# Performance work log

Measured on AMD Instinct MI355X. Metric: run time of the kernel, lower is better.

Reference implementation:

```python
import jax, jax.numpy as jnp
import numpy as np

N_NODES = 100000
N_EDGES = 1600000
NFEAT, NHID, NCLASS = 512, 128, 16


def gcn_conv(x, edge_index, edge_weight, W, b):
    # Dense linear transform: [N, in] @ [in, out] -> [N, out]
    h = x @ W
    src, dst = edge_index[0], edge_index[1]
    # Edge-weighted gather + scatter-add (message passing)
    msgs = edge_weight[:, None] * h[src]            # [E, out]
    agg = jax.ops.segment_sum(msgs, dst, num_segments=x.shape[0])
    return agg + b


def setup_inputs() -> dict:
    key = jax.random.key(0)
    k = jax.random.split(key, 8)
    x = jax.random.normal(k[0], (N_NODES, NFEAT), dtype=jnp.float32)
    edge_index = jax.random.randint(k[1], (2, N_EDGES), 0, N_NODES, dtype=jnp.int64 if jax.config.jax_enable_x64 else jnp.int32)
    edge_weight = jax.random.uniform(k[2], (N_EDGES,), dtype=jnp.float32)
    # GCNConv glorot-initialized weights + zero biases
    s1 = np.sqrt(6.0 / (NFEAT + NHID)).astype(np.float32)
    s2 = np.sqrt(6.0 / (NHID + NCLASS)).astype(np.float32)
    W1 = jax.random.uniform(k[3], (NFEAT, NHID), minval=-s1, maxval=s1, dtype=jnp.float32)
    b1 = jnp.zeros((NHID,), dtype=jnp.float32)
    W2 = jax.random.uniform(k[4], (NHID, NCLASS), minval=-s2, maxval=s2, dtype=jnp.float32)
    b2 = jnp.zeros((NCLASS,), dtype=jnp.float32)
    return {"x": x, "edge_index": edge_index, "edge_weight": edge_weight,
            "W1": W1, "b1": b1, "W2": W2, "b2": b2}


def reference(x, edge_index, edge_weight, W1, b1, W2, b2):
    # GNNGuard.forward in eval mode (dropout is identity when not training)
    h = jax.nn.relu(gcn_conv(x, edge_index, edge_weight, W1, b1))
    out = gcn_conv(h, edge_index, edge_weight, W2, b2)
    return jax.nn.log_softmax(out, axis=1)
```

## Files before the change

### kernel.cpp

```cpp
#include <hip/hip_runtime.h>
#include <cstdint>
#include <cstddef>


#define NFEAT 512
#define NHID 128
#define NCLASS 16
#define MAXDEG 64

typedef __attribute__((ext_vector_type(8))) __bf16 bf16x8;
typedef __attribute__((ext_vector_type(4))) float f32x4;

__global__ void k_prep_w1(const float* __restrict__ W1, __bf16* __restrict__ W1f) {
    int t = blockIdx.x * 256 + threadIdx.x;
    if (t >= 16 * 8 * 64) return;
    int lane = t & 63;
    int nc = (t >> 6) & 7;
    int ks = t >> 9;
    int q = lane >> 4, col = lane & 15;
    __bf16* outp = W1f + (size_t)t * 8;
#pragma unroll
    for (int j = 0; j < 8; j++) {
        int k = ks * 32 + q * 8 + j;
        int n = nc * 16 + col;
        outp[j] = (__bf16)W1[k * NHID + n];
    }
}

__global__ void k_gemm1_scatter(const float* __restrict__ x, const __bf16* __restrict__ W1f,
                                __bf16* __restrict__ h1b, int M, int nG1,
                                const int* __restrict__ src, const int* __restrict__ dst,
                                const float* __restrict__ ew, int* __restrict__ cnt,
                                int2* __restrict__ pay, int E) {
    if ((int)blockIdx.x >= nG1) {
        int e = (blockIdx.x - nG1) * 256 + threadIdx.x;
        if (e < E) {
            int d = dst[e];
            int r = atomicAdd(&cnt[d], 1);
            if (r < MAXDEG) {
                int2 pv;
                pv.x = src[e];
                pv.y = __float_as_int(ew[e]);
                pay[(size_t)d * MAXDEG + r] = pv;
            }
        }
        return;
    }
    int wave = threadIdx.x >> 6;
    int lane = threadIdx.x & 63;
    int q = lane >> 4;
    int col = lane & 15;
    int m0 = blockIdx.x * 64 + wave * 16 + col;
    bool valid = (m0 < M);

    f32x4 acc[8];
#pragma unroll
    for (int n = 0; n < 8; n++) acc[n] = (f32x4)(0.0f);

    const bf16x8* Bf = (const bf16x8*)W1f;
    const float* arow = x + (size_t)m0 * NFEAT + q * 8;

    for (int kk = 0; kk < NFEAT; kk += 32) {
        bf16x8 af;
        if (valid) {
            const f32x4* ap = (const f32x4*)(arow + kk);
            f32x4 a0 = __builtin_nontemporal_load(ap);
            f32x4 a1 = __builtin_nontemporal_load(ap + 1);
            af[0] = (__bf16)a0[0]; af[1] = (__bf16)a0[1];
            af[2] = (__bf16)a0[2]; af[3] = (__bf16)a0[3];
            af[4] = (__bf16)a1[0]; af[5] = (__bf16)a1[1];
            af[6] = (__bf16)a1[2]; af[7] = (__bf16)a1[3];
        } else {
#pragma unroll
            for (int j = 0; j < 8; j++) af[j] = (__bf16)0.0f;
        }
        int kb = (kk >> 5) * 8;
#pragma unroll
        for (int n = 0; n < 8; n++) {
            bf16x8 bf = Bf[(size_t)(kb + n) * 64 + lane];
            acc[n] = __builtin_amdgcn_mfma_f32_16x16x32_bf16(af, bf, acc[n], 0, 0, 0);
        }
    }

    int rbase = blockIdx.x * 64 + wave * 16 + q * 4;
#pragma unroll
    for (int r = 0; r < 4; r++) {
        int row = rbase + r;
        if (row < M) {
            __bf16* op = h1b + (size_t)row * NHID + col;
#pragma unroll
            for (int n = 0; n < 8; n++) op[n * 16] = (__bf16)acc[n][r];
        }
    }
}

__global__ void k_agg1(const uint32_t* __restrict__ h1u, const int* __restrict__ cnt,
                       const int2* __restrict__ pay, const float* __restrict__ b1,
                       uint32_t* __restrict__ hu, int N) {
    int gw = (blockIdx.x * 256 + (int)threadIdx.x) >> 6;
    int lane = threadIdx.x & 63;
    if (gw >= N) return;
    int c = cnt[gw];
    if (c > MAXDEG) c = MAXDEG;
    const int2* prow = pay + (size_t)gw * MAXDEG;
    int sv = 0;
    float wv = 0.f;
    if (lane < c) {
        int2 pv = prow[lane];
        sv = pv.x;
        wv = __int_as_float(pv.y);
    }
    float ax = 0.f, ay = 0.f;
    int j = 0;
    for (; j + 4 <= c; j += 4) {
        int s0 = __shfl(sv, j + 0), s1 = __shfl(sv, j + 1);
        int s2 = __shfl(sv, j + 2), s3 = __shfl(sv, j + 3);
        float w0 = __shfl(wv, j + 0), w1 = __shfl(wv, j + 1);
        float w2 = __shfl(wv, j + 2), w3 = __shfl(wv, j + 3);
        uint32_t u0 = h1u[(size_t)s0 * 64 + lane];
        uint32_t u1 = h1u[(size_t)s1 * 64 + lane];
        uint32_t u2 = h1u[(size_t)s2 * 64 + lane];
        uint32_t u3 = h1u[(size_t)s3 * 64 + lane];
        ax = fmaf(w0, __uint_as_float(u0 << 16), ax);
        ay = fmaf(w0, __uint_as_float(u0 & 0xffff0000u), ay);
        ax = fmaf(w1, __uint_as_float(u1 << 16), ax);
        ay = fmaf(w1, __uint_as_float(u1 & 0xffff0000u), ay);
        ax = fmaf(w2, __uint_as_float(u2 << 16), ax);
        ay = fmaf(w2, __uint_as_float(u2 & 0xffff0000u), ay);
        ax = fmaf(w3, __uint_as_float(u3 << 16), ax);
        ay = fmaf(w3, __uint_as_float(u3 & 0xffff0000u), ay);
    }
    for (; j < c; j++) {
        int s = __shfl(sv, j);
        float ww = __shfl(wv, j);
        uint32_t u = h1u[(size_t)s * 64 + lane];
        ax = fmaf(ww, __uint_as_float(u << 16), ax);
        ay = fmaf(ww, __uint_as_float(u & 0xffff0000u), ay);
    }
    float2 bb = ((const float2*)b1)[lane];
    float ox = fmaxf(ax + bb.x, 0.f);
    float oy = fmaxf(ay + bb.y, 0.f);
    union { __bf16 h[2]; uint32_t u; } cvt;
    cvt.h[0] = (__bf16)ox;
    cvt.h[1] = (__bf16)oy;
    hu[(size_t)gw * 64 + lane] = cvt.u;
}

__global__ void k_gemm2(const uint32_t* __restrict__ hu, const float* __restrict__ W2,
                        float* __restrict__ h2, int N) {
    __shared__ float W2s[NHID * NCLASS];
    __shared__ float hs[16][NHID + 4];
    int t = threadIdx.x;
#pragma unroll
    for (int j = 0; j < 8; j++) W2s[t * 8 + j] = W2[t * 8 + j];
    int nb = blockIdx.x * 16;
    {
        int idx = t * 4;
        int row = idx >> 6;
        int kp = idx & 63;
        if (nb + row < N) {
            uint4 u4 = *(const uint4*)(hu + (size_t)(nb + row) * 64 + kp);
            uint32_t us[4] = {u4.x, u4.y, u4.z, u4.w};
#pragma unroll
            for (int j = 0; j < 4; j++) {
                hs[row][(kp + j) * 2 + 0] = __uint_as_float(us[j] << 16);
                hs[row][(kp + j) * 2 + 1] = __uint_as_float(us[j] & 0xffff0000u);
            }
        } else {
#pragma unroll
            for (int j = 0; j < 4; j++) {
                hs[row][(kp + j) * 2 + 0] = 0.f;
                hs[row][(kp + j) * 2 + 1] = 0.f;
            }
        }
    }
    __syncthreads();
    int ni = t >> 4, c = t & 15;
    float acc = 0.f;
#pragma unroll 8
    for (int k = 0; k < NHID; k++) acc = fmaf(hs[ni][k], W2s[k * NCLASS + c], acc);
    if (nb + ni < N) h2[(size_t)(nb + ni) * NCLASS + c] = acc;
}

__global__ void k_agg2(const float* __restrict__ h2, const int* __restrict__ cnt,
                       const int2* __restrict__ pay, const float* __restrict__ b2,
                       float* __restrict__ out, int N) {
    int t = blockIdx.x * 256 + threadIdx.x;
    int node = t >> 4;
    int c = t & 15;
    if (node >= N) return;
    int n = cnt[node];
    if (n > MAXDEG) n = MAXDEG;
    const int2* prow = pay + (size_t)node * MAXDEG;
    float acc = 0.f;
    int j = 0;
    for (; j + 4 <= n; j += 4) {
        int2 p0 = prow[j + 0];
        int2 p1 = prow[j + 1];
        int2 p2 = prow[j + 2];
        int2 p3 = prow[j + 3];
        float v0 = h2[(size_t)p0.x * NCLASS + c];
        float v1 = h2[(size_t)p1.x * NCLASS + c];
        float v2 = h2[(size_t)p2.x * NCLASS + c];
        float v3 = h2[(size_t)p3.x * NCLASS + c];
        acc = fmaf(__int_as_float(p0.y), v0, acc);
        acc = fmaf(__int_as_float(p1.y), v1, acc);
        acc = fmaf(__int_as_float(p2.y), v2, acc);
        acc = fmaf(__int_as_float(p3.y), v3, acc);
    }
    for (; j < n; j++) {
        int2 pv = prow[j];
        acc = fmaf(__int_as_float(pv.y), h2[(size_t)pv.x * NCLASS + c], acc);
    }
    float o = acc + b2[c];
    float m = o;
#pragma unroll
    for (int d = 1; d < 16; d <<= 1) m = fmaxf(m, __shfl_xor(m, d));
    float e = expf(o - m);
    float ssum = e;
#pragma unroll
    for (int d = 1; d < 16; d <<= 1) ssum += __shfl_xor(ssum, d);
    out[(size_t)node * NCLASS + c] = o - m - logf(ssum);
}

extern "C" void kernel_launch(void* const* d_in, const int* in_sizes, int n_in,
                              void* d_out, int out_size, void* d_ws, size_t ws_size,
                              hipStream_t stream) {
    const float* x  = (const float*)d_in[0];
    const int*   ei = (const int*)d_in[1];
    const float* ew = (const float*)d_in[2];
    const float* W1 = (const float*)d_in[3];
    const float* b1 = (const float*)d_in[4];
    const float* W2 = (const float*)d_in[5];
    const float* b2 = (const float*)d_in[6];
    float* out = (float*)d_out;

    int N = in_sizes[0] / NFEAT;
    int E = in_sizes[2];
    const int* srcI = ei;
    const int* dstI = ei + E;

    char* p = (char*)d_ws;
    auto alloc = [&](size_t bytes) {
        char* r = p;
        p += (bytes + 511) & ~(size_t)511;
        return r;
    };
    __bf16*   h1b  = (__bf16*)alloc((size_t)N * NHID * 2);
    uint32_t* hu   = (uint32_t*)alloc((size_t)N * (NHID / 2) * 4);
    float*    h2   = (float*)alloc((size_t)N * NCLASS * 4);
    int*      cnt  = (int*)alloc((size_t)N * 4);
    int2*     pay  = (int2*)alloc((size_t)N * MAXDEG * 8);
    __bf16*   W1f  = (__bf16*)alloc((size_t)NFEAT * NHID * 2);

    (void)hipMemsetAsync(cnt, 0, (size_t)N * 4, stream);
    k_prep_w1<<<32, 256, 0, stream>>>(W1, W1f);

    int nG1 = (N + 63) / 64;
    int nSc = (E + 255) / 256;
    k_gemm1_scatter<<<nG1 + nSc, 256, 0, stream>>>(x, W1f, h1b, N, nG1,
                                                   srcI, dstI, ew, cnt, pay, E);

    k_agg1<<<(N + 3) / 4, 256, 0, stream>>>((const uint32_t*)h1b, cnt, pay, b1, hu, N);
    k_gemm2<<<(N + 15) / 16, 256, 0, stream>>>(hu, W2, h2, N);
    k_agg2<<<(int)(((size_t)N * 16 + 255) / 256), 256, 0, stream>>>(h2, cnt, pay, b2, out, N);
}
```

Before: 495.5 us.

## Pad degree counters, widen GEMM tile, reorder blocks, restructure aggregation kernels

Measured after the change: 542.8 us. 1.1x slower.

```diff
diff --git a/kernel.cpp b/kernel.cpp
--- a/kernel.cpp
+++ b/kernel.cpp
@@ -7,6 +7,7 @@
 #define NHID 128
 #define NCLASS 16
 #define MAXDEG 64
+#define CNTPAD 16
 
 typedef __attribute__((ext_vector_type(8))) __bf16 bf16x8;
 typedef __attribute__((ext_vector_type(4))) float f32x4;
@@ -28,15 +29,15 @@
 }
 
 __global__ void k_gemm1_scatter(const float* __restrict__ x, const __bf16* __restrict__ W1f,
-                                __bf16* __restrict__ h1b, int M, int nG1,
+                                __bf16* __restrict__ h1b, int M, int nSc,
                                 const int* __restrict__ src, const int* __restrict__ dst,
                                 const float* __restrict__ ew, int* __restrict__ cnt,
                                 int2* __restrict__ pay, int E) {
-    if ((int)blockIdx.x >= nG1) {
-        int e = (blockIdx.x - nG1) * 256 + threadIdx.x;
+    if ((int)blockIdx.x < nSc) {
+        int e = blockIdx.x * 256 + threadIdx.x;
         if (e < E) {
             int d = dst[e];
-            int r = atomicAdd(&cnt[d], 1);
+            int r = atomicAdd(&cnt[(size_t)d * CNTPAD], 1);
             if (r < MAXDEG) {
                 int2 pv;
                 pv.x = src[e];
@@ -46,50 +47,72 @@
         }
         return;
     }
+    int bid = blockIdx.x - nSc;
     int wave = threadIdx.x >> 6;
     int lane = threadIdx.x & 63;
     int q = lane >> 4;
     int col = lane & 15;
-    int m0 = blockIdx.x * 64 + wave * 16 + col;
-    bool valid = (m0 < M);
-
-    f32x4 acc[8];
-#pragma unroll
-    for (int n = 0; n < 8; n++) acc[n] = (f32x4)(0.0f);
+    int rowbase = bid * 128 + wave * 32;
+    int m0 = rowbase + col;
+    int m1 = rowbase + 16 + col;
+    bool v0 = (m0 < M), v1 = (m1 < M);
+
+    f32x4 acc[2][8];
+#pragma unroll
+    for (int f = 0; f < 2; f++)
+#pragma unroll
+        for (int n = 0; n < 8; n++) acc[f][n] = (f32x4)(0.0f);
 
     const bf16x8* Bf = (const bf16x8*)W1f;
-    const float* arow = x + (size_t)m0 * NFEAT + q * 8;
+    const float* arow0 = x + (size_t)m0 * NFEAT + q * 8;
+    const float* arow1 = x + (size_t)m1 * NFEAT + q * 8;
 
     for (int kk = 0; kk < NFEAT; kk += 32) {
-        bf16x8 af;
-        if (valid) {
-            const f32x4* ap = (const f32x4*)(arow + kk);
+        bf16x8 af0, af1;
+        if (v0) {
+            const f32x4* ap = (const f32x4*)(arow0 + kk);
             f32x4 a0 = __builtin_nontemporal_load(ap);
             f32x4 a1 = __builtin_nontemporal_load(ap + 1);
-            af[0] = (__bf16)a0[0]; af[1] = (__bf16)a0[1];
-            af[2] = (__bf16)a0[2]; af[3] = (__bf16)a0[3];
-            af[4] = (__bf16)a1[0]; af[5] = (__bf16)a1[1];
-            af[6] = (__bf16)a1[2]; af[7] = (__bf16)a1[3];
+            af0[0] = (__bf16)a0[0]; af0[1] = (__bf16)a0[1];
+            af0[2] = (__bf16)a0[2]; af0[3] = (__bf16)a0[3];
+            af0[4] = (__bf16)a1[0]; af0[5] = (__bf16)a1[1];
+            af0[6] = (__bf16)a1[2]; af0[7] = (__bf16)a1[3];
         } else {
 #pragma unroll
-            for (int j = 0; j < 8; j++) af[j] = (__bf16)0.0f;
+            for (int j = 0; j < 8; j++) af0[j] = (__bf16)0.0f;
+        }
+        if (v1) {
+            const f32x4* ap = (const f32x4*)(arow1 + kk);
+            f32x4 a0 = __builtin_nontemporal_load(ap);
+            f32x4 a1 = __builtin_nontemporal_load(ap + 1);
+            af1[0] = (__bf16)a0[0]; af1[1] = (__bf16)a0[1];
+            af1[2] = (__bf16)a0[2]; af1[3] = (__bf16)a0[3];
+            af1[4] = (__bf16)a1[0]; af1[5] = (__bf16)a1[1];
+            af1[6] = (__bf16)a1[2]; af1[7] = (__bf16)a1[3];
+        } else {
+#pragma unroll
+            for (int j = 0; j < 8; j++) af1[j] = (__bf16)0.0f;
         }
         int kb = (kk >> 5) * 8;
 #pragma unroll
         for (int n = 0; n < 8; n++) {
             bf16x8 bf = Bf[(size_t)(kb + n) * 64 + lane];
-            acc[n] = __builtin_amdgcn_mfma_f32_16x16x32_bf16(af, bf, acc[n], 0, 0, 0);
-        }
-    }
-
-    int rbase = blockIdx.x * 64 + wave * 16 + q * 4;
-#pragma unroll
-    for (int r = 0; r < 4; r++) {
-        int row = rbase + r;
-        if (row < M) {
-            __bf16* op = h1b + (size_t)row * NHID + col;
-#pragma unroll
-            for (int n = 0; n < 8; n++) op[n * 16] = (__bf16)acc[n][r];
+            acc[0][n] = __builtin_amdgcn_mfma_f32_16x16x32_bf16(af0, bf, acc[0][n], 0, 0, 0);
+            acc[1][n] = __builtin_amdgcn_mfma_f32_16x16x32_bf16(af1, bf, acc[1][n], 0, 0, 0);
+        }
+    }
+
+#pragma unroll
+    for (int f = 0; f < 2; f++) {
+        int rb = rowbase + f * 16 + q * 4;
+#pragma unroll
+        for (int r = 0; r < 4; r++) {
+            int row = rb + r;
+            if (row < M) {
+                __bf16* op = h1b + (size_t)row * NHID + col;
+#pragma unroll
+                for (int n = 0; n < 8; n++) op[n * 16] = (__bf16)acc[f][n][r];
+            }
         }
     }
 }
@@ -100,7 +123,7 @@
     int gw = (blockIdx.x * 256 + (int)threadIdx.x) >> 6;
     int lane = threadIdx.x & 63;
     if (gw >= N) return;
-    int c = cnt[gw];
+    int c = cnt[(size_t)gw * CNTPAD];
     if (c > MAXDEG) c = MAXDEG;
     const int2* prow = pay + (size_t)gw * MAXDEG;
     int sv = 0;
@@ -112,23 +135,35 @@
     }
     float ax = 0.f, ay = 0.f;
     int j = 0;
+    for (; j + 8 <= c; j += 8) {
+        uint32_t u[8];
+        float w[8];
+#pragma unroll
+        for (int i = 0; i < 8; i++) {
+            int s = __shfl(sv, j + i);
+            w[i] = __shfl(wv, j + i);
+            u[i] = h1u[(size_t)s * 64 + lane];
+        }
+#pragma unroll
+        for (int i = 0; i < 8; i++) {
+            ax = fmaf(w[i], __uint_as_float(u[i] << 16), ax);
+            ay = fmaf(w[i], __uint_as_float(u[i] & 0xffff0000u), ay);
+        }
+    }
     for (; j + 4 <= c; j += 4) {
-        int s0 = __shfl(sv, j + 0), s1 = __shfl(sv, j + 1);
-        int s2 = __shfl(sv, j + 2), s3 = __shfl(sv, j + 3);
-        float w0 = __shfl(wv, j + 0), w1 = __shfl(wv, j + 1);
-        float w2 = __shfl(wv, j + 2), w3 = __shfl(wv, j + 3);
-        uint32_t u0 = h1u[(size_t)s0 * 64 + lane];
-        uint32_t u1 = h1u[(size_t)s1 * 64 + lane];
-        uint32_t u2 = h1u[(size_t)s2 * 64 + lane];
-        uint32_t u3 = h1u[(size_t)s3 * 64 + lane];
-        ax = fmaf(w0, __uint_as_float(u0 << 16), ax);
-        ay = fmaf(w0, __uint_as_float(u0 & 0xffff0000u), ay);
-        ax = fmaf(w1, __uint_as_float(u1 << 16), ax);
-        ay = fmaf(w1, __uint_as_float(u1 & 0xffff0000u), ay);
-        ax = fmaf(w2, __uint_as_float(u2 << 16), ax);
-        ay = fmaf(w2, __uint_as_float(u2 & 0xffff0000u), ay);
-        ax = fmaf(w3, __uint_as_float(u3 << 16), ax);
-        ay = fmaf(w3, __uint_as_float(u3 & 0xffff0000u), ay);
+        uint32_t u[4];
+        float w[4];
+#pragma unroll
+        for (int i = 0; i < 4; i++) {
+            int s = __shfl(sv, j + i);
+            w[i] = __shfl(wv, j + i);
+            u[i] = h1u[(size_t)s * 64 + lane];
+        }
+#pragma unroll
+        for (int i = 0; i < 4; i++) {
+            ax = fmaf(w[i], __uint_as_float(u[i] << 16), ax);
+            ay = fmaf(w[i], __uint_as_float(u[i] & 0xffff0000u), ay);
+        }
     }
     for (; j < c; j++) {
         int s = __shfl(sv, j);
@@ -185,33 +220,40 @@
 __global__ void k_agg2(const float* __restrict__ h2, const int* __restrict__ cnt,
                        const int2* __restrict__ pay, const float* __restrict__ b2,
                        float* __restrict__ out, int N) {
-    int t = blockIdx.x * 256 + threadIdx.x;
-    int node = t >> 4;
-    int c = t & 15;
-    if (node >= N) return;
-    int n = cnt[node];
+    int gw = (blockIdx.x * 256 + (int)threadIdx.x) >> 6;
+    int lane = threadIdx.x & 63;
+    if (gw >= N) return;
+    int c = lane & 15, eg = lane >> 4;
+    int n = cnt[(size_t)gw * CNTPAD];
     if (n > MAXDEG) n = MAXDEG;
-    const int2* prow = pay + (size_t)node * MAXDEG;
+    const int2* prow = pay + (size_t)gw * MAXDEG;
+    int sv = 0;
+    float wv = 0.f;
+    if (lane < n) {
+        int2 pv = prow[lane];
+        sv = pv.x;
+        wv = __int_as_float(pv.y);
+    }
     float acc = 0.f;
-    int j = 0;
-    for (; j + 4 <= n; j += 4) {
-        int2 p0 = prow[j + 0];
-        int2 p1 = prow[j + 1];
-        int2 p2 = prow[j + 2];
-        int2 p3 = prow[j + 3];
-        float v0 = h2[(size_t)p0.x * NCLASS + c];
-        float v1 = h2[(size_t)p1.x * NCLASS + c];
-        float v2 = h2[(size_t)p2.x * NCLASS + c];
-        float v3 = h2[(size_t)p3.x * NCLASS + c];
-        acc = fmaf(__int_as_float(p0.y), v0, acc);
-        acc = fmaf(__int_as_float(p1.y), v1, acc);
-        acc = fmaf(__int_as_float(p2.y), v2, acc);
-        acc = fmaf(__int_as_float(p3.y), v3, acc);
-    }
-    for (; j < n; j++) {
-        int2 pv = prow[j];
-        acc = fmaf(__int_as_float(pv.y), h2[(size_t)pv.x * NCLASS + c], acc);
-    }
+    int nr = (n + 3) >> 2;
+    int i = 0;
+    for (; i + 2 <= nr; i += 2) {
+        int j0 = i * 4 + eg, j1 = j0 + 4;
+        int s0 = __shfl(sv, j0), s1 = __shfl(sv, j1);
+        float w0 = __shfl(wv, j0), w1 = __shfl(wv, j1);
+        float g0 = h2[(size_t)s0 * NCLASS + c];
+        float g1 = h2[(size_t)s1 * NCLASS + c];
+        acc = fmaf(w0, g0, acc);
+        acc = fmaf(w1, g1, acc);
+    }
+    if (i < nr) {
+        int j0 = i * 4 + eg;
+        int s0 = __shfl(sv, j0);
+        float w0 = __shfl(wv, j0);
+        acc = fmaf(w0, h2[(size_t)s0 * NCLASS + c], acc);
+    }
+    acc += __shfl_xor(acc, 16);
+    acc += __shfl_xor(acc, 32);
     float o = acc + b2[c];
     float m = o;
 #pragma unroll
@@ -220,7 +262,7 @@
     float ssum = e;
 #pragma unroll
     for (int d = 1; d < 16; d <<= 1) ssum += __shfl_xor(ssum, d);
-    out[(size_t)node * NCLASS + c] = o - m - logf(ssum);
+    if (lane < 16) out[(size_t)gw * NCLASS + c] = o - m - logf(ssum);
 }
 
 extern "C" void kernel_launch(void* const* d_in, const int* in_sizes, int n_in,
@@ -249,19 +291,19 @@
     __bf16*   h1b  = (__bf16*)alloc((size_t)N * NHID * 2);
     uint32_t* hu   = (uint32_t*)alloc((size_t)N * (NHID / 2) * 4);
     float*    h2   = (float*)alloc((size_t)N * NCLASS * 4);
-    int*      cnt  = (int*)alloc((size_t)N * 4);
+    int*      cnt  = (int*)alloc((size_t)N * CNTPAD * 4);
     int2*     pay  = (int2*)alloc((size_t)N * MAXDEG * 8);
     __bf16*   W1f  = (__bf16*)alloc((size_t)NFEAT * NHID * 2);
 
-    (void)hipMemsetAsync(cnt, 0, (size_t)N * 4, stream);
+    (void)hipMemsetAsync(cnt, 0, (size_t)N * CNTPAD * 4, stream);
     k_prep_w1<<<32, 256, 0, stream>>>(W1, W1f);
 
-    int nG1 = (N + 63) / 64;
+    int nG1 = (N + 127) / 128;
     int nSc = (E + 255) / 256;
-    k_gemm1_scatter<<<nG1 + nSc, 256, 0, stream>>>(x, W1f, h1b, N, nG1,
+    k_gemm1_scatter<<<nSc + nG1, 256, 0, stream>>>(x, W1f, h1b, N, nSc,
                                                    srcI, dstI, ew, cnt, pay, E);
 
     k_agg1<<<(N + 3) / 4, 256, 0, stream>>>((const uint32_t*)h1b, cnt, pay, b1, hu, N);
     k_gemm2<<<(N + 15) / 16, 256, 0, stream>>>(hu, W2, h2, N);
-    k_agg2<<<(int)(((size_t)N * 16 + 255) / 256), 256, 0, stream>>>(h2, cnt, pay, b2, out, N);
-}
+    k_agg2<<<(N + 3) / 4, 256, 0, stream>>>(h2, cnt, pay, b2, out, N);
+}
```
